# Kernel tuning notes

Measured on AMD Instinct MI355X. Metric: run time of the kernel, lower is better.

## Reference

```python
import jax, jax.numpy as jnp
import numpy as np

EMBED_DIM = 768
NUM_HEADS = 12
LORA_DIM = 64
HEAD_DIM = EMBED_DIM // NUM_HEADS
SCALING = float(HEAD_DIM) ** -0.5


def quick_gelu(x):
    return x * jax.nn.sigmoid(1.702 * x)


def setup_inputs() -> dict:
    key = jax.random.key(0)
    ks = jax.random.split(key, 12)
    bsz, tgt_len, E = 128, 197, EMBED_DIM
    x = jax.random.normal(ks[0], (bsz, tgt_len, E), dtype=jnp.float32)
    attn_mask = jnp.zeros((bsz, tgt_len, tgt_len), dtype=jnp.float32)
    top_idx = jax.random.randint(ks[1], (bsz,), 0, tgt_len)
    s = 0.02
    return {
        "x": x,
        "attn_mask": attn_mask,
        "in_proj_weight": jax.random.normal(ks[2], (3 * E, E)) * s,
        "in_proj_bias": jnp.zeros((3 * E,), jnp.float32),
        "out_proj_weight": jax.random.normal(ks[3], (E, E)) * s,
        "out_proj_bias": jnp.zeros((E,), jnp.float32),
        "lora_a": jax.random.normal(ks[4], (LORA_DIM, E)) * s,
        "lora_b": jax.random.normal(ks[5], (3 * E, LORA_DIM)) * s,
        "down_weight": jax.random.normal(ks[6], (LORA_DIM, E)) * s,
        "down_bias": jax.random.normal(ks[7], (LORA_DIM,)) * 1e-6,
        "up_weight": jax.random.normal(ks[8], (E, LORA_DIM)) * s,
        "up_bias": jnp.zeros((E,), jnp.float32),
        "n_f": 16,
        "top_idx": top_idx,
    }


def reference(x, attn_mask, in_proj_weight, in_proj_bias, out_proj_weight,
              out_proj_bias, lora_a, lora_b, down_weight, down_bias,
              up_weight, up_bias, n_f, top_idx):
    bsz, tgt_len, E = x.shape
    H, hd = NUM_HEADS, HEAD_DIM
    b = bsz // n_f

    # fused QKV + LoRA delta
    qkv = x @ in_proj_weight.T + in_proj_bias          # [bsz, L, 3E]
    qkv = qkv + (x @ lora_a.T) @ lora_b.T              # LoRA delta
    qkv = qkv.reshape(bsz, tgt_len, 3, H, hd)
    qkv = jnp.transpose(qkv, (2, 0, 3, 1, 4))          # [3, bsz, H, L, hd]
    q, k, v = qkv[0], qkv[1], qkv[2]

    # gather per-sample CLS query before scaling (matches torch order)
    q_1 = q[jnp.arange(bsz), :, top_idx, :]            # [bsz, H, hd]
    q_1 = jnp.transpose(q_1.reshape(b, n_f, H, hd), (0, 2, 1, 3))  # [b, H, f, hd]

    # frame-local attention
    attn = jnp.einsum('bhqd,bhkd->bhqk', q * SCALING, k) + attn_mask[:, None, :, :]
    attn = jax.nn.softmax(attn, axis=-1)
    xo = jnp.einsum('bhqk,bhkd->bhqd', attn, v)
    xo = jnp.transpose(xo, (0, 2, 1, 3)).reshape(bsz, tgt_len, E)
    xo = xo @ out_proj_weight.T + out_proj_bias        # [bsz, L, E]

    # global CLS attention over all frames' keys/values
    k_g = jnp.transpose(k.reshape(b, n_f, H, tgt_len, hd), (0, 2, 1, 3, 4)).reshape(b, H, n_f * tgt_len, hd)
    v_g = jnp.transpose(v.reshape(b, n_f, H, tgt_len, hd), (0, 2, 1, 3, 4)).reshape(b, H, n_f * tgt_len, hd)
    mask_g = attn_mask[:, -1, :].reshape(b, n_f * tgt_len)  # [b, f*L]

    attn_1 = jnp.einsum('bhfd,bhkd->bhfk', q_1 * SCALING, k_g) + mask_g[:, None, None, :]
    attn_1 = jax.nn.softmax(attn_1, axis=-1)
    x_1 = jnp.einsum('bhfk,bhkd->bhfd', attn_1, v_g)
    x_1 = jnp.transpose(x_1, (0, 2, 1, 3)).reshape(b, n_f, E)
    x_1 = x_1 @ out_proj_weight.T + out_proj_bias      # [b, f, E]

    # adapter on gathered CLS outputs
    x_0 = xo[jnp.arange(bsz), top_idx, :].reshape(b, n_f, E)
    x_0 = quick_gelu(x_0 @ down_weight.T + down_bias)
    x_0 = x_0 @ up_weight.T + up_bias                  # [b, f, E]

    update_cls = (x_0 + x_1).reshape(bsz, E)
    xo = xo.at[jnp.arange(bsz), top_idx, :].set(update_cls)
    return xo
```

## Files before the change

kernel.cpp:

```cpp
#include <hip/hip_runtime.h>
#include <hip/hip_bf16.h>

typedef __attribute__((ext_vector_type(4))) float f32x4;
typedef __attribute__((ext_vector_type(8))) short s16x8;

#define BSZ 128
#define TGT 197
#define EDIM 768
#define NH 12
#define HD 64
#define NF 16
#define M_TOT (BSZ*TGT)
#define QKV_N (3*EDIM)
#define KG (NF*TGT)
#define KGP 3328
#define VSTR 264

__device__ __forceinline__ float b2f(unsigned short u) {
  return __uint_as_float(((unsigned int)u) << 16);
}
__device__ __forceinline__ float bf2f(__hip_bfloat16 b) { return __bfloat162float(b); }
__device__ __forceinline__ __hip_bfloat16 f2bf(float f) { return __float2bfloat16(f); }
__device__ __forceinline__ unsigned int packbf(float a, float b) {
  __hip_bfloat16 x = __float2bfloat16(a), y = __float2bfloat16(b);
  return (unsigned int)*(unsigned short*)&x | ((unsigned int)*(unsigned short*)&y << 16);
}
__device__ __forceinline__ int swz(int t, int c) {
  return t*64 + (c ^ ((((t & 7) ^ ((t >> 3) & 3))) << 3));
}
__device__ __forceinline__ int vswz(int d, int t) {
  return d*VSTR + (t ^ (d & 56));
}

__device__ __forceinline__ void gload_lds16(const void* gsrc, void* ldst) {
  __builtin_amdgcn_global_load_lds(
      (const __attribute__((address_space(1))) unsigned int*)gsrc,
      (__attribute__((address_space(3))) unsigned int*)ldst, 16, 0, 0);
}

__global__ void detect_dtype(const unsigned short* __restrict__ xraw,
                             int* __restrict__ flag, int* __restrict__ mz) {
  if (threadIdx.x == 0 && blockIdx.x == 0) {
    float mx = 0.f;
    for (int j = 0; j < 1024; ++j) {
      float v = fabsf(b2f(xraw[j]));
      if (v < 1e30f) mx = fmaxf(mx, v);
      else mx = 1e30f;
    }
    *flag = (mx < 100.0f) ? 1 : 0;
    *mz = 1;
  }
}

__global__ __launch_bounds__(256) void detect_mask_zero(
    const unsigned int* __restrict__ mraw, int nelem,
    const int* __restrict__ flag, int* __restrict__ mz)
{
  const int isbf = *flag;
  const int nwords = isbf ? (nelem >> 1) : nelem;
  const unsigned int am = isbf ? 0x7fff7fffu : 0x7fffffffu;
  unsigned int acc = 0;
  for (int i = blockIdx.x*256 + threadIdx.x; i < nwords; i += gridDim.x*256)
    acc |= (mraw[i] & am);
  if (acc) atomicAnd(mz, 0);
}

__global__ __launch_bounds__(256) void convert_bf16(
    const void* __restrict__ src, __hip_bfloat16* __restrict__ dst,
    int n8, const int* __restrict__ flag, int skip_if_bf)
{
  const int isbf = *flag;
  if (skip_if_bf && isbf) return;
  int i = blockIdx.x * 256 + threadIdx.x;
  const int stride = gridDim.x * 256;
  if (isbf) {
    const s16x8* s = (const s16x8*)src;
    s16x8* d = (s16x8*)dst;
    for (; i < n8; i += stride) d[i] = s[i];
  } else {
    const f32x4* s = (const f32x4*)src;
    s16x8* d = (s16x8*)dst;
    for (; i < n8; i += stride) {
      f32x4 a = s[i*2], b = s[i*2+1];
      s16x8 o;
      #pragma unroll
      for (int j = 0; j < 4; ++j) { __hip_bfloat16 t = f2bf(a[j]); o[j] = *(short*)&t; }
      #pragma unroll
      for (int j = 0; j < 4; ++j) { __hip_bfloat16 t = f2bf(b[j]); o[4+j] = *(short*)&t; }
      d[i] = o;
    }
  }
}

struct CvBatch {
  const void* src[10];
  void* dst[10];
  int off8[11];
};

__global__ __launch_bounds__(256) void convert_batch(CvBatch cb, const int* __restrict__ flag)
{
  const int isbf = *flag;
  const int total = cb.off8[10];
  for (int i = blockIdx.x*256 + threadIdx.x; i < total; i += gridDim.x*256) {
    int s = 0;
    #pragma unroll
    for (int k = 1; k < 10; ++k) s += (i >= cb.off8[k]);
    const int li = i - cb.off8[s];
    if (isbf) {
      ((s16x8*)cb.dst[s])[li] = ((const s16x8*)cb.src[s])[li];
    } else {
      const f32x4* sp = (const f32x4*)cb.src[s];
      f32x4 a = sp[li*2], b = sp[li*2+1];
      s16x8 o;
      #pragma unroll
      for (int j = 0; j < 4; ++j) { __hip_bfloat16 t = f2bf(a[j]); o[j] = *(short*)&t; }
      #pragma unroll
      for (int j = 0; j < 4; ++j) { __hip_bfloat16 t = f2bf(b[j]); o[4+j] = *(short*)&t; }
      ((s16x8*)cb.dst[s])[li] = o;
    }
  }
}

__global__ __launch_bounds__(256) void build_wc(
    const __hip_bfloat16* __restrict__ W,
    const __hip_bfloat16* __restrict__ la,
    const __hip_bfloat16* __restrict__ lb,
    __hip_bfloat16* __restrict__ Wc)
{
  __shared__ float lbr[64];
  const int n = blockIdx.x;
  if (threadIdx.x < 64) lbr[threadIdx.x] = bf2f(lb[n*64 + threadIdx.x]);
  __syncthreads();
  for (int e = threadIdx.x; e < EDIM; e += 256) {
    float acc = bf2f(W[(size_t)n*EDIM + e]);
    for (int r = 0; r < 64; ++r) acc += lbr[r] * bf2f(la[r*EDIM + e]);
    Wc[(size_t)n*EDIM + e] = f2bf(acc);
  }
}

__global__ __launch_bounds__(512) void gemm_bt_8ph(
    const __hip_bfloat16* __restrict__ A,
    const __hip_bfloat16* __restrict__ A_alt,
    const __hip_bfloat16* __restrict__ B,
    const __hip_bfloat16* __restrict__ bias,
    void* __restrict__ C,
    int M, int N, int K, int ntiles,
    const int* __restrict__ flag, int flag_mode)
{
  __shared__ char lds[131072];
  const int tid = threadIdx.x;
  const int wave = tid >> 6, lane = tid & 63;
  const int l16 = lane & 15, kq = lane >> 4;
  const int wr = wave >> 2, wc2 = wave & 3;

  const int nwg = gridDim.x;
  const int bid = blockIdx.x;
  const int qc = nwg >> 3, rc = nwg & 7;
  const int xcd = bid & 7;
  const int wgid = (xcd < rc ? xcd*(qc+1) : rc*(qc+1) + (xcd-rc)*qc) + (bid >> 3);
  const long brow = (long)(wgid / ntiles) * 256;
  const long bcol = (long)(wgid % ntiles) * 256;

  const int isbf = *flag;
  const __hip_bfloat16* Ause = isbf ? A_alt : A;
  const int nkt = K >> 6;

  const int srow = tid >> 3;
  const int schunk = tid & 7;
  const int wuni = wave << 10;

  auto stA = [&](int t, int buf, int issue) {
    int ar = issue*64 + srow;
    int cs = schunk ^ (ar & 7);
    long gr = brow + ar; if (gr > (long)M - 1) gr = M - 1;
    gload_lds16(Ause + gr*(long)K + t*64 + cs*8,
                lds + buf*65536 + issue*8192 + wuni);
  };
  auto stB = [&](int t, int buf, int issue) {
    int br = issue*64 + srow;
    int cs = schunk ^ (br & 7);
    gload_lds16(B + (bcol + br)*(long)K + t*64 + cs*8,
                lds + buf*65536 + 32768 + issue*8192 + wuni);
  };
  auto rdA = [&](int buf, int q, int a, int ks) -> s16x8 {
    int ar = wr*128 + q*32 + a*16 + l16;
    int ch = ks*4 + kq;
    return *(const s16x8*)(lds + buf*65536 + ar*128 + ((ch ^ (ar & 7)) << 4));
  };
  auto rdB = [&](int buf, int ni, int ks) -> s16x8 {
    int br = wc2*64 + ni*16 + l16;
    int ch = ks*4 + kq;
    return *(const s16x8*)(lds + buf*65536 + 32768 + br*128 + ((ch ^ (br & 7)) << 4));
  };

  f32x4 acc[8][4];
  #pragma unroll
  for (int i = 0; i < 8; ++i)
    #pragma unroll
    for (int j = 0; j < 4; ++j) acc[i][j] = (f32x4){0.f,0.f,0.f,0.f};

  stB(0,0,0); stB(0,0,1); stB(0,0,2); stB(0,0,3);
  stA(0,0,0); stA(0,0,2); stA(0,0,1); stA(0,0,3);
  asm volatile("s_waitcnt vmcnt(2)" ::: "memory");
  __builtin_amdgcn_s_barrier();

  for (int t = 0; t < nkt; ++t) {
    const int cur = t & 1, nxt = cur ^ 1;
    const bool pf = (t + 1 < nkt);
    s16x8 bfr[4][2], af[2][2];

    #pragma unroll
    for (int ni = 0; ni < 4; ++ni) { bfr[ni][0] = rdB(cur,ni,0); bfr[ni][1] = rdB(cur,ni,1); }
    af[0][0]=rdA(cur,0,0,0); af[0][1]=rdA(cur,0,0,1);
    af[1][0]=rdA(cur,0,1,0); af[1][1]=rdA(cur,0,1,1);
    if (pf) {
      stB(t+1,nxt,0); stB(t+1,nxt,1); stB(t+1,nxt,2); stB(t+1,nxt,3);
      stA(t+1,nxt,0); stA(t+1,nxt,2); stA(t+1,nxt,1); stA(t+1,nxt,3);
    }
    __builtin_amdgcn_s_barrier();
    asm volatile("s_waitcnt lgkmcnt(0)" ::: "memory");
    __builtin_amdgcn_sched_barrier(0);
    __builtin_amdgcn_s_setprio(1);
    #pragma unroll
    for (int ks = 0; ks < 2; ++ks)
      #pragma unroll
      for (int ni = 0; ni < 4; ++ni) {
        acc[0][ni] = __builtin_amdgcn_mfma_f32_16x16x32_bf16(af[0][ks], bfr[ni][ks], acc[0][ni], 0,0,0);
        acc[1][ni] = __builtin_amdgcn_mfma_f32_16x16x32_bf16(af[1][ks], bfr[ni][ks], acc[1][ni], 0,0,0);
      }
    __builtin_amdgcn_s_setprio(0);

    af[0][0]=rdA(cur,1,0,0); af[0][1]=rdA(cur,1,0,1);
    af[1][0]=rdA(cur,1,1,0); af[1][1]=rdA(cur,1,1,1);
    if (pf) asm volatile("s_waitcnt vmcnt(8)" ::: "memory");
    else    asm volatile("s_waitcnt vmcnt(0)" ::: "memory");
    __builtin_amdgcn_s_barrier();
    asm volatile("s_waitcnt lgkmcnt(0)" ::: "memory");
    __builtin_amdgcn_sched_barrier(0);
    __builtin_amdgcn_s_setprio(1);
    #pragma unroll
    for (int ks = 0; ks < 2; ++ks)
      #pragma unroll
      for (int ni = 0; ni < 4; ++ni) {
        acc[2][ni] = __builtin_amdgcn_mfma_f32_16x16x32_bf16(af[0][ks], bfr[ni][ks], acc[2][ni], 0,0,0);
        acc[3][ni] = __builtin_amdgcn_mfma_f32_16x16x32_bf16(af[1][ks], bfr[ni][ks], acc[3][ni], 0,0,0);
      }
    __builtin_amdgcn_s_setprio(0);

    af[0][0]=rdA(cur,2,0,0); af[0][1]=rdA(cur,2,0,1);
    af[1][0]=rdA(cur,2,1,0); af[1][1]=rdA(cur,2,1,1);
    __builtin_amdgcn_s_barrier();
    asm volatile("s_waitcnt lgkmcnt(0)" ::: "memory");
    __builtin_amdgcn_sched_barrier(0);
    __builtin_amdgcn_s_setprio(1);
    #pragma unroll
    for (int ks = 0; ks < 2; ++ks)
      #pragma unroll
      for (int ni = 0; ni < 4; ++ni) {
        acc[4][ni] = __builtin_amdgcn_mfma_f32_16x16x32_bf16(af[0][ks], bfr[ni][ks], acc[4][ni], 0,0,0);
        acc[5][ni] = __builtin_amdgcn_mfma_f32_16x16x32_bf16(af[1][ks], bfr[ni][ks], acc[5][ni], 0,0,0);
      }
    __builtin_amdgcn_s_setprio(0);

    af[0][0]=rdA(cur,3,0,0); af[0][1]=rdA(cur,3,0,1);
    af[1][0]=rdA(cur,3,1,0); af[1][1]=rdA(cur,3,1,1);
    if (pf) asm volatile("s_waitcnt vmcnt(2)" ::: "memory");
    __builtin_amdgcn_s_barrier();
    asm volatile("s_waitcnt lgkmcnt(0)" ::: "memory");
    __builtin_amdgcn_sched_barrier(0);
    __builtin_amdgcn_s_setprio(1);
    #pragma unroll
    for (int ks = 0; ks < 2; ++ks)
      #pragma unroll
      for (int ni = 0; ni < 4; ++ni) {
        acc[6][ni] = __builtin_amdgcn_mfma_f32_16x16x32_bf16(af[0][ks], bfr[ni][ks], acc[6][ni], 0,0,0);
        acc[7][ni] = __builtin_amdgcn_mfma_f32_16x16x32_bf16(af[1][ks], bfr[ni][ks], acc[7][ni], 0,0,0);
      }
    __builtin_amdgcn_s_setprio(0);
  }

  __builtin_amdgcn_s_barrier();

  const int f32o = flag_mode && (!isbf);
  float bv[4];
  #pragma unroll
  for (int ni = 0; ni < 4; ++ni) bv[ni] = bf2f(bias[bcol + wc2*64 + ni*16 + l16]);
  const int o4 = kq*4;

  if (!f32o) {
    __hip_bfloat16* eb = (__hip_bfloat16*)(lds + wave*2048);
    __hip_bfloat16* Cb = (__hip_bfloat16*)C;
    const int rr = lane >> 3, cg = lane & 7;
    #pragma unroll
    for (int mi = 0; mi < 8; ++mi) {
      #pragma unroll
      for (int ni = 0; ni < 4; ++ni)
        #pragma unroll
        for (int r = 0; r < 4; ++r) {
          const int row16 = o4 + r;
          const int sidx = row16*64 + ((((ni*2 + (l16 >> 3)) ^ (row16 & 7)) << 3) | (l16 & 7));
          eb[sidx] = f2bf(acc[mi][ni][r] + bv[ni]);
        }
      asm volatile("s_waitcnt lgkmcnt(0)" ::: "memory");
      __builtin_amdgcn_sched_barrier(0);
      #pragma unroll
      for (int pass = 0; pass < 2; ++pass) {
        const int row16 = pass*8 + rr;
        const long grow = brow + wr*128 + mi*16 + row16;
        if (grow < M) {
          s16x8 v = *(const s16x8*)(eb + row16*64 + ((cg ^ (row16 & 7)) << 3));
          *(s16x8*)(Cb + grow*(long)N + bcol + wc2*64 + cg*8) = v;
        }
      }
      asm volatile("s_waitcnt lgkmcnt(0)" ::: "memory");
      __builtin_amdgcn_sched_barrier(0);
    }
  } else {
    #pragma unroll
    for (int mi = 0; mi < 8; ++mi)
      #pragma unroll
      for (int ni = 0; ni < 4; ++ni)
        #pragma unroll
        for (int r = 0; r < 4; ++r) {
          const long grow = brow + wr*128 + mi*16 + o4 + r;
          if (grow < M)
            ((float*)C)[grow*(long)N + bcol + wc2*64 + ni*16 + l16] = acc[mi][ni][r] + bv[ni];
        }
  }
}

__global__ __launch_bounds__(256) void attn_fused(
    const __hip_bfloat16* __restrict__ qkv,
    const __hip_bfloat16* __restrict__ mask,
    const __hip_bfloat16* __restrict__ mask_raw,
    const int* __restrict__ flag,
    const int* __restrict__ mzp,
    __hip_bfloat16* __restrict__ xop)
{
  __shared__ __hip_bfloat16 lVt[64*VSTR];

  const int tid = threadIdx.x;
  const int blk = blockIdx.x;
  const int xcd = blk & 7;
  const int slot = blk >> 3;
  const int ih = xcd * 192 + (slot >> 2);
  const int qt = slot & 3;
  const int h = ih % NH;
  const int i = ih / NH;
  const int q0 = qt * 64;
  const size_t rowbase = (size_t)i * TGT;
  const int wave = tid >> 6, lane = tid & 63;
  const int l16 = lane & 15, kq = lane >> 4;
  const int mz = *mzp;
  const __hip_bfloat16* msk = (*flag) ? mask_raw : mask;

  int qr = q0 + wave*16 + l16;
  const int qrc = qr > TGT-1 ? TGT-1 : qr;
  s16x8 qf[2];
  #pragma unroll
  for (int kk = 0; kk < 2; ++kk)
    qf[kk] = *(const s16x8*)(qkv + (rowbase + qrc)*QKV_N + h*HD + kk*32 + kq*8);

  const f32x4 z = {0.f,0.f,0.f,0.f};
  for (int idx = tid; idx < 224*8; idx += 256) {
    int t = idx >> 3, c8 = idx & 7;
    f32x4 vv = z;
    if (t < TGT) vv = *(const f32x4*)(qkv + (rowbase + t)*QKV_N + 2*EDIM + h*HD + c8*8);
    const __hip_bfloat16* pv = (const __hip_bfloat16*)&vv;
    const int tx = t ^ (c8 << 3);
    #pragma unroll
    for (int j = 0; j < 8; ++j)
      lVt[(c8*8 + j)*VSTR + tx] = pv[j];
  }
  __syncthreads();

  f32x4 acc[14];
  #pragma unroll
  for (int nf = 0; nf < 14; ++nf) {
    int trow = nf*16 + l16; if (trow > TGT-1) trow = TGT-1;
    acc[nf] = (f32x4){0.f,0.f,0.f,0.f};
    #pragma unroll
    for (int kk = 0; kk < 2; ++kk) {
      s16x8 kf = *(const s16x8*)(qkv + (rowbase + trow)*QKV_N + EDIM + h*HD + kk*32 + kq*8);
      acc[nf] = __builtin_amdgcn_mfma_f32_16x16x32_bf16(kf, qf[kk], acc[nf], 0, 0, 0);
    }
  }

  float mx = -1e30f;
  #pragma unroll
  for (int nf = 0; nf < 14; ++nf) {
    #pragma unroll
    for (int r = 0; r < 4; ++r) {
      const int t = nf*16 + kq*4 + r;
      float s;
      if (t < TGT) {
        s = acc[nf][r]*0.125f;
        if (!mz) s += bf2f(msk[(rowbase + qrc)*TGT + t]);
      } else s = -1e30f;
      acc[nf][r] = s;
      mx = fmaxf(mx, s);
    }
  }
  mx = fmaxf(mx, __shfl_xor(mx, 16));
  mx = fmaxf(mx, __shfl_xor(mx, 32));

  float rs = 0.f;
  unsigned int pk[14][2];
  #pragma unroll
  for (int nf = 0; nf < 14; ++nf) {
    float p0 = __expf(acc[nf][0] - mx);
    float p1 = __expf(acc[nf][1] - mx);
    float p2 = __expf(acc[nf][2] - mx);
    float p3 = __expf(acc[nf][3] - mx);
    rs += (p0 + p1) + (p2 + p3);
    pk[nf][0] = packbf(p0, p1);
    pk[nf][1] = packbf(p2, p3);
  }
  rs += __shfl_xor(rs, 16);
  rs += __shfl_xor(rs, 32);

  f32x4 oacc[4];
  #pragma unroll
  for (int nf = 0; nf < 4; ++nf) oacc[nf] = (f32x4){0.f,0.f,0.f,0.f};

  const int slbase = l16 + ((kq & 1) << 5);
  #pragma unroll
  for (int kt = 0; kt < 7; ++kt) {
    s16x8 pa;
    #pragma unroll
    for (int jp = 0; jp < 4; ++jp) {
      const int srcLane = slbase + ((jp >> 1) << 4);
      int va = __shfl((int)pk[2*kt][jp & 1], srcLane, 64);
      int vb = __shfl((int)pk[2*kt + 1][jp & 1], srcLane, 64);
      int sel = (kq < 2) ? va : vb;
      pa[2*jp]     = (short)(sel & 0xffff);
      pa[2*jp + 1] = (short)(((unsigned int)sel) >> 16);
    }
    #pragma unroll
    for (int nf = 0; nf < 4; ++nf) {
      s16x8 vf = *(const s16x8*)(lVt + vswz(nf*16 + l16, kt*32 + kq*8));
      oacc[nf] = __builtin_amdgcn_mfma_f32_16x16x32_bf16(pa, vf, oacc[nf], 0, 0, 0);
    }
  }

  #pragma unroll
  for (int r = 0; r < 4; ++r) {
    const float rsrc = __shfl(rs, kq*4 + r, 64);
    const int qw = q0 + wave*16 + kq*4 + r;
    if (qw < TGT) {
      const float inv = 1.0f / rsrc;
      #pragma unroll
      for (int nf = 0; nf < 4; ++nf)
        xop[(rowbase + qw)*(size_t)EDIM + h*HD + nf*16 + l16] = f2bf(oacc[nf][r] * inv);
    }
  }
}

__global__ __launch_bounds__(256) void cls_attn(
    const __hip_bfloat16* __restrict__ qkv,
    const __hip_bfloat16* __restrict__ mask,
    const __hip_bfloat16* __restrict__ mask_raw,
    const int* __restrict__ flag,
    const int* __restrict__ mzp,
    const int* __restrict__ top_idx,
    __hip_bfloat16* __restrict__ Sg_all,
    __hip_bfloat16* __restrict__ x1buf)
{
  __shared__ __hip_bfloat16 lQ[16*64];
  __shared__ __hip_bfloat16 lV[256*64];
  __shared__ float red[16][17];
  __shared__ float rmax[16];
  __shared__ float rsum[16];

  const int tid = threadIdx.x;
  const int g = blockIdx.x / NH;
  const int h = blockIdx.x % NH;
  __hip_bfloat16* Sg = Sg_all + (size_t)blockIdx.x * 16 * KGP;
  const int wave = tid >> 6, lane = tid & 63;
  const int l16 = lane & 15, kq = lane >> 4, o4 = (lane >> 4) * 4;
  const int mz = *mzp;
  const __hip_bfloat16* msk = (*flag) ? mask_raw : mask;

  if (tid < 128) {
    int qi = tid >> 3, c8 = tid & 7;
    int ib = g*NF + qi;
    int top = top_idx[ib];
    f32x4 v = *(const f32x4*)(qkv + ((size_t)ib*TGT + top)*QKV_N + h*HD + c8*8);
    *(f32x4*)(lQ + qi*64 + c8*8) = v;
  }
  __syncthreads();

  s16x8 q8[2];
  #pragma unroll
  for (int kk = 0; kk < 2; ++kk)
    q8[kk] = *(const s16x8*)(lQ + l16*64 + kk*32 + kq*8);

  for (int nf = wave; nf < 208; nf += 4) {
    const int key = nf*16 + l16;
    if (nf < 197) {
      f32x4 a = {0.f,0.f,0.f,0.f};
      const size_t krow = (size_t)g*KG + key;
      #pragma unroll
      for (int kk = 0; kk < 2; ++kk) {
        s16x8 k8 = *(const s16x8*)(qkv + krow*QKV_N + EDIM + h*HD + kk*32 + kq*8);
        a = __builtin_amdgcn_mfma_f32_16x16x32_bf16(q8[kk], k8, a, 0, 0, 0);
      }
      float mval = 0.f;
      if (!mz) {
        const int f = key / 197;
        const int t = key - f*197;
        mval = bf2f(msk[((size_t)(g*NF + f)*TGT + (TGT-1))*TGT + t]);
      }
      #pragma unroll
      for (int r = 0; r < 4; ++r)
        Sg[(o4 + r)*KGP + key] = f2bf(a[r]*0.125f + mval);
    } else {
      #pragma unroll
      for (int r = 0; r < 4; ++r)
        Sg[(o4 + r)*KGP + key] = f2bf(0.f);
    }
  }
  __syncthreads();

  {
    const int q = tid >> 4, c = tid & 15;
    float mx = -1e30f;
    for (int gch = c; gch < 394; gch += 16) {
      s16x8 sv = *(const s16x8*)(Sg + q*KGP + gch*8);
      #pragma unroll
      for (int j = 0; j < 8; ++j) mx = fmaxf(mx, b2f((unsigned short)sv[j]));
    }
    red[q][c] = mx;
    __syncthreads();
    if (tid < 16) {
      float m = red[tid][0];
      for (int j = 1; j < 16; ++j) m = fmaxf(m, red[tid][j]);
      rmax[tid] = m;
    }
    __syncthreads();
    const float rowmax = rmax[q];
    float sum = 0.f;
    for (int gch = c; gch < 394; gch += 16) {
      s16x8 sv = *(const s16x8*)(Sg + q*KGP + gch*8);
      s16x8 ov;
      #pragma unroll
      for (int jp = 0; jp < 4; ++jp) {
        float e0 = __expf(b2f((unsigned short)sv[2*jp])   - rowmax);
        float e1 = __expf(b2f((unsigned short)sv[2*jp+1]) - rowmax);
        sum += e0 + e1;
        unsigned int pr = packbf(e0, e1);
        ov[2*jp]   = (short)(pr & 0xffff);
        ov[2*jp+1] = (short)(pr >> 16);
      }
      *(s16x8*)(Sg + q*KGP + gch*8) = ov;
    }
    red[q][c] = sum;
    __syncthreads();
    if (tid < 16) {
      float s = 0.f;
      for (int j = 0; j < 16; ++j) s += red[tid][j];
      rsum[tid] = s;
    }
  }

  f32x4 oa = {0.f,0.f,0.f,0.f};
  const f32x4 z = {0.f,0.f,0.f,0.f};
  for (int ck = 0; ck < KGP; ck += 256) {
    __syncthreads();
    for (int idx = tid; idx < 256*8; idx += 256) {
      int t2 = idx >> 3, c8 = idx & 7;
      int key = ck + t2;
      f32x4 v = z;
      if (key < KG) v = *(const f32x4*)(qkv + ((size_t)g*KG + key)*QKV_N + 2*EDIM + h*HD + c8*8);
      *(f32x4*)(lV + swz(t2, c8*8)) = v;
    }
    __syncthreads();
    #pragma unroll
    for (int ks = 0; ks < 8; ++ks) {
      s16x8 pa = *(const s16x8*)(Sg + l16*KGP + ck + ks*32 + kq*8);
      s16x8 vf;
      #pragma unroll
      for (int j = 0; j < 8; ++j) {
        const int t2 = ks*32 + kq*8 + j;
        vf[j] = *(const short*)(lV + swz(t2, wave*16 + l16));
      }
      oa = __builtin_amdgcn_mfma_f32_16x16x32_bf16(pa, vf, oa, 0, 0, 0);
    }
  }
  #pragma unroll
  for (int r = 0; r < 4; ++r) {
    int q = o4 + r;
    int ib = g*NF + q;
    x1buf[(size_t)ib*EDIM + h*HD + wave*16 + l16] = f2bf(oa[r] / rsum[q]);
  }
}

__global__ __launch_bounds__(256) void final_update(
    void* __restrict__ out,
    const __hip_bfloat16* __restrict__ x1p,
    const __hip_bfloat16* __restrict__ dw, const __hip_bfloat16* __restrict__ db,
    const __hip_bfloat16* __restrict__ uw, const __hip_bfloat16* __restrict__ ub,
    const int* __restrict__ top_idx, const int* __restrict__ flag)
{
  __shared__ float x0[EDIM];
  __shared__ float hmid[64];
  const int i = blockIdx.x;
  const int tid = threadIdx.x;
  const int top = top_idx[i];
  const int isbf = *flag;
  const size_t rowoff = ((size_t)i*TGT + top)*EDIM;
  for (int e = tid; e < EDIM; e += 256)
    x0[e] = isbf ? bf2f(((const __hip_bfloat16*)out)[rowoff + e])
                 : ((const float*)out)[rowoff + e];
  __syncthreads();
  if (tid < 64) {
    float a = bf2f(db[tid]);
    for (int e = 0; e < EDIM; ++e) a += x0[e] * bf2f(dw[tid*EDIM + e]);
    hmid[tid] = a / (1.f + __expf(-1.702f * a));
  }
  __syncthreads();
  for (int e = tid; e < EDIM; e += 256) {
    float a = bf2f(ub[e]) + bf2f(x1p[(size_t)i*EDIM + e]);
    #pragma unroll
    for (int r = 0; r < 64; ++r) a += hmid[r] * bf2f(uw[e*64 + r]);
    if (isbf) ((__hip_bfloat16*)out)[rowoff + e] = f2bf(a);
    else ((float*)out)[rowoff + e] = a;
  }
}

extern "C" void kernel_launch(void* const* d_in, const int* in_sizes, int n_in,
                              void* d_out, int out_size, void* d_ws, size_t ws_size,
                              hipStream_t stream) {
  (void)in_sizes; (void)n_in; (void)out_size; (void)ws_size;
  const int* top_idx = (const int*)d_in[13];
  const __hip_bfloat16* x_raw    = (const __hip_bfloat16*)d_in[0];
  const __hip_bfloat16* mask_raw = (const __hip_bfloat16*)d_in[1];

  char* ws = (char*)d_ws;
  size_t off = 0;
  auto alloc = [&](size_t bytes) { char* p = ws + off; off += (bytes + 15) & ~(size_t)15; return p; };

  int* flag = (int*)alloc(16);
  int* mz   = (int*)alloc(16);
  __hip_bfloat16* x_c    = (__hip_bfloat16*)alloc((size_t)19365888*2);
  __hip_bfloat16* mask_c = (__hip_bfloat16*)alloc((size_t)4967552*2);
  __hip_bfloat16* wIn_c  = (__hip_bfloat16*)alloc((size_t)1769472*2);
  __hip_bfloat16* bIn_c  = (__hip_bfloat16*)alloc((size_t)2304*2);
  __hip_bfloat16* wOut_c = (__hip_bfloat16*)alloc((size_t)589824*2);
  __hip_bfloat16* bOut_c = (__hip_bfloat16*)alloc((size_t)768*2);
  __hip_bfloat16* la_c   = (__hip_bfloat16*)alloc((size_t)49152*2);
  __hip_bfloat16* lb_c   = (__hip_bfloat16*)alloc((size_t)147456*2);
  __hip_bfloat16* dw_c   = (__hip_bfloat16*)alloc((size_t)49152*2);
  __hip_bfloat16* db_c   = (__hip_bfloat16*)alloc((size_t)64*2);
  __hip_bfloat16* uw_c   = (__hip_bfloat16*)alloc((size_t)49152*2);
  __hip_bfloat16* ub_c   = (__hip_bfloat16*)alloc((size_t)768*2);
  __hip_bfloat16* Wc     = (__hip_bfloat16*)alloc((size_t)QKV_N*EDIM*2);
  __hip_bfloat16* qkv    = (__hip_bfloat16*)alloc((size_t)M_TOT*QKV_N*2);
  __hip_bfloat16* xop    = (__hip_bfloat16*)alloc((size_t)M_TOT*EDIM*2);
  __hip_bfloat16* x1b    = (__hip_bfloat16*)alloc((size_t)BSZ*EDIM*2);
  __hip_bfloat16* x1p    = (__hip_bfloat16*)alloc((size_t)BSZ*EDIM*2);
  __hip_bfloat16* Sg     = (__hip_bfloat16*)alloc((size_t)96*16*KGP*2);

  detect_dtype<<<1, 64, 0, stream>>>((const unsigned short*)d_in[0], flag, mz);
  detect_mask_zero<<<2048, 256, 0, stream>>>((const unsigned int*)d_in[1], 4967552, flag, mz);

  convert_bf16<<<2048, 256, 0, stream>>>(d_in[0], x_c, 19365888/8, flag, 1);
  convert_bf16<<<2048, 256, 0, stream>>>(d_in[1], mask_c, 4967552/8, flag, 1);

  CvBatch cb;
  const int srcIdx[10] = {2,3,4,5,6,7,8,9,10,11};
  void* dsts[10] = {wIn_c, bIn_c, wOut_c, bOut_c, la_c, lb_c, dw_c, db_c, uw_c, ub_c};
  const int ns[10] = {1769472, 2304, 589824, 768, 49152, 147456, 49152, 64, 49152, 768};
  int cum = 0;
  for (int k = 0; k < 10; ++k) {
    cb.src[k] = d_in[srcIdx[k]];
    cb.dst[k] = dsts[k];
    cb.off8[k] = cum;
    cum += ns[k] / 8;
  }
  cb.off8[10] = cum;
  convert_batch<<<(cum + 255)/256, 256, 0, stream>>>(cb, flag);

  build_wc<<<2304, 256, 0, stream>>>(wIn_c, la_c, lb_c, Wc);

  gemm_bt_8ph<<<99*9, 512, 0, stream>>>(x_c, x_raw, Wc, bIn_c, qkv,
                                        M_TOT, QKV_N, EDIM, 9, flag, 0);
  attn_fused<<<dim3(6144), 256, 0, stream>>>(qkv, mask_c, mask_raw, flag, mz, xop);
  gemm_bt_8ph<<<99*3, 512, 0, stream>>>(xop, xop, wOut_c, bOut_c, d_out,
                                        M_TOT, EDIM, EDIM, 3, flag, 1);
  cls_attn<<<dim3(96), 256, 0, stream>>>(qkv, mask_c, mask_raw, flag, mz, top_idx, Sg, x1b);
  gemm_bt_8ph<<<1*3, 512, 0, stream>>>(x1b, x1b, wOut_c, bOut_c, x1p,
                                       BSZ, EDIM, EDIM, 3, flag, 0);
  final_update<<<128, 256, 0, stream>>>(d_out, x1p, dw_c, db_c, uw_c, ub_c, top_idx, flag);
}
```

Before: 561.9 us.

## Split CLS global attention across key chunks and stagger GEMM prefetch loads

The global CLS attention, previously 96 blocks each scanning 3152 keys through a global scratch score buffer, is split into 8 key chunks per (group, head). Each chunk keeps its scores in LDS and writes partial max/sum/output, and a new combine kernel merges them flash-decoding style. This raises parallelism from 96 to 768 blocks and removes the global Sg round-trip, at the cost of an extra launch and partial buffers. Separately, the GEMM main loop now spreads its next-tile global-to-LDS loads across the four phases and adjusts the vmcnt waits accordingly.

Result: faster. 469.9 us (-16.4%).

```diff
diff --git a/kernel.cpp b/kernel.cpp
--- a/kernel.cpp
+++ b/kernel.cpp
@@ -13,8 +13,10 @@
 #define M_TOT (BSZ*TGT)
 #define QKV_N (3*EDIM)
 #define KG (NF*TGT)
-#define KGP 3328
 #define VSTR 264
+#define NSPL 8
+#define KSPL 394
+#define LSTR 424
 
 __device__ __forceinline__ float b2f(unsigned short u) {
   return __uint_as_float(((unsigned int)u) << 16);
@@ -214,10 +216,7 @@
     for (int ni = 0; ni < 4; ++ni) { bfr[ni][0] = rdB(cur,ni,0); bfr[ni][1] = rdB(cur,ni,1); }
     af[0][0]=rdA(cur,0,0,0); af[0][1]=rdA(cur,0,0,1);
     af[1][0]=rdA(cur,0,1,0); af[1][1]=rdA(cur,0,1,1);
-    if (pf) {
-      stB(t+1,nxt,0); stB(t+1,nxt,1); stB(t+1,nxt,2); stB(t+1,nxt,3);
-      stA(t+1,nxt,0); stA(t+1,nxt,2); stA(t+1,nxt,1); stA(t+1,nxt,3);
-    }
+    if (pf) { stB(t+1,nxt,0); stB(t+1,nxt,1); }
     __builtin_amdgcn_s_barrier();
     asm volatile("s_waitcnt lgkmcnt(0)" ::: "memory");
     __builtin_amdgcn_sched_barrier(0);
@@ -233,8 +232,12 @@
 
     af[0][0]=rdA(cur,1,0,0); af[0][1]=rdA(cur,1,0,1);
     af[1][0]=rdA(cur,1,1,0); af[1][1]=rdA(cur,1,1,1);
-    if (pf) asm volatile("s_waitcnt vmcnt(8)" ::: "memory");
-    else    asm volatile("s_waitcnt vmcnt(0)" ::: "memory");
+    if (pf) {
+      stB(t+1,nxt,2); stB(t+1,nxt,3);
+      asm volatile("s_waitcnt vmcnt(4)" ::: "memory");
+    } else {
+      asm volatile("s_waitcnt vmcnt(0)" ::: "memory");
+    }
     __builtin_amdgcn_s_barrier();
     asm volatile("s_waitcnt lgkmcnt(0)" ::: "memory");
     __builtin_amdgcn_sched_barrier(0);
@@ -250,6 +253,7 @@
 
     af[0][0]=rdA(cur,2,0,0); af[0][1]=rdA(cur,2,0,1);
     af[1][0]=rdA(cur,2,1,0); af[1][1]=rdA(cur,2,1,1);
+    if (pf) { stA(t+1,nxt,0); stA(t+1,nxt,2); }
     __builtin_amdgcn_s_barrier();
     asm volatile("s_waitcnt lgkmcnt(0)" ::: "memory");
     __builtin_amdgcn_sched_barrier(0);
@@ -265,7 +269,8 @@
 
     af[0][0]=rdA(cur,3,0,0); af[0][1]=rdA(cur,3,0,1);
     af[1][0]=rdA(cur,3,1,0); af[1][1]=rdA(cur,3,1,1);
-    if (pf) asm volatile("s_waitcnt vmcnt(2)" ::: "memory");
+    if (pf) { stA(t+1,nxt,1); stA(t+1,nxt,3); }
+    asm volatile("s_waitcnt vmcnt(2)" ::: "memory");
     __builtin_amdgcn_s_barrier();
     asm volatile("s_waitcnt lgkmcnt(0)" ::: "memory");
     __builtin_amdgcn_sched_barrier(0);
@@ -457,26 +462,30 @@
   }
 }
 
-__global__ __launch_bounds__(256) void cls_attn(
+__global__ __launch_bounds__(256) void cls_split(
     const __hip_bfloat16* __restrict__ qkv,
     const __hip_bfloat16* __restrict__ mask,
     const __hip_bfloat16* __restrict__ mask_raw,
     const int* __restrict__ flag,
     const int* __restrict__ mzp,
     const int* __restrict__ top_idx,
-    __hip_bfloat16* __restrict__ Sg_all,
-    __hip_bfloat16* __restrict__ x1buf)
+    float* __restrict__ pO,
+    float* __restrict__ pm,
+    float* __restrict__ pl)
 {
   __shared__ __hip_bfloat16 lQ[16*64];
+  __shared__ __hip_bfloat16 lS[16*LSTR];
   __shared__ __hip_bfloat16 lV[256*64];
   __shared__ float red[16][17];
   __shared__ float rmax[16];
   __shared__ float rsum[16];
 
   const int tid = threadIdx.x;
-  const int g = blockIdx.x / NH;
-  const int h = blockIdx.x % NH;
-  __hip_bfloat16* Sg = Sg_all + (size_t)blockIdx.x * 16 * KGP;
+  const int sp = blockIdx.x & 7;
+  const int gh = blockIdx.x >> 3;
+  const int g = gh / NH;
+  const int h = gh % NH;
+  const int k0 = sp * KSPL;
   const int wave = tid >> 6, lane = tid & 63;
   const int l16 = lane & 15, kq = lane >> 4, o4 = (lane >> 4) * 4;
   const int mz = *mzp;
@@ -496,38 +505,33 @@
   for (int kk = 0; kk < 2; ++kk)
     q8[kk] = *(const s16x8*)(lQ + l16*64 + kk*32 + kq*8);
 
-  for (int nf = wave; nf < 208; nf += 4) {
-    const int key = nf*16 + l16;
-    if (nf < 197) {
-      f32x4 a = {0.f,0.f,0.f,0.f};
-      const size_t krow = (size_t)g*KG + key;
-      #pragma unroll
-      for (int kk = 0; kk < 2; ++kk) {
-        s16x8 k8 = *(const s16x8*)(qkv + krow*QKV_N + EDIM + h*HD + kk*32 + kq*8);
-        a = __builtin_amdgcn_mfma_f32_16x16x32_bf16(q8[kk], k8, a, 0, 0, 0);
-      }
-      float mval = 0.f;
-      if (!mz) {
-        const int f = key / 197;
-        const int t = key - f*197;
-        mval = bf2f(msk[((size_t)(g*NF + f)*TGT + (TGT-1))*TGT + t]);
-      }
-      #pragma unroll
-      for (int r = 0; r < 4; ++r)
-        Sg[(o4 + r)*KGP + key] = f2bf(a[r]*0.125f + mval);
-    } else {
-      #pragma unroll
-      for (int r = 0; r < 4; ++r)
-        Sg[(o4 + r)*KGP + key] = f2bf(0.f);
-    }
+  for (int nf = wave; nf < 26; nf += 4) {
+    const int keyl = nf*16 + l16;
+    const int keyg = k0 + (keyl < KSPL ? keyl : 0);
+    f32x4 a = {0.f,0.f,0.f,0.f};
+    const size_t krow = (size_t)g*KG + keyg;
+    #pragma unroll
+    for (int kk = 0; kk < 2; ++kk) {
+      s16x8 k8 = *(const s16x8*)(qkv + krow*QKV_N + EDIM + h*HD + kk*32 + kq*8);
+      a = __builtin_amdgcn_mfma_f32_16x16x32_bf16(q8[kk], k8, a, 0, 0, 0);
+    }
+    float mval = 0.f;
+    if (!mz && keyl < KSPL) {
+      const int f = keyg / 197;
+      const int t = keyg - f*197;
+      mval = bf2f(msk[((size_t)(g*NF + f)*TGT + (TGT-1))*TGT + t]);
+    }
+    #pragma unroll
+    for (int r = 0; r < 4; ++r)
+      lS[(o4 + r)*LSTR + nf*16 + l16] = f2bf(keyl < KSPL ? a[r]*0.125f + mval : -1e30f);
   }
   __syncthreads();
 
   {
     const int q = tid >> 4, c = tid & 15;
     float mx = -1e30f;
-    for (int gch = c; gch < 394; gch += 16) {
-      s16x8 sv = *(const s16x8*)(Sg + q*KGP + gch*8);
+    for (int gch = c; gch < 52; gch += 16) {
+      s16x8 sv = *(const s16x8*)(lS + q*LSTR + gch*8);
       #pragma unroll
       for (int j = 0; j < 8; ++j) mx = fmaxf(mx, b2f((unsigned short)sv[j]));
     }
@@ -541,8 +545,8 @@
     __syncthreads();
     const float rowmax = rmax[q];
     float sum = 0.f;
-    for (int gch = c; gch < 394; gch += 16) {
-      s16x8 sv = *(const s16x8*)(Sg + q*KGP + gch*8);
+    for (int gch = c; gch < 52; gch += 16) {
+      s16x8 sv = *(const s16x8*)(lS + q*LSTR + gch*8);
       s16x8 ov;
       #pragma unroll
       for (int jp = 0; jp < 4; ++jp) {
@@ -553,7 +557,7 @@
         ov[2*jp]   = (short)(pr & 0xffff);
         ov[2*jp+1] = (short)(pr >> 16);
       }
-      *(s16x8*)(Sg + q*KGP + gch*8) = ov;
+      *(s16x8*)(lS + q*LSTR + gch*8) = ov;
     }
     red[q][c] = sum;
     __syncthreads();
@@ -566,19 +570,23 @@
 
   f32x4 oa = {0.f,0.f,0.f,0.f};
   const f32x4 z = {0.f,0.f,0.f,0.f};
-  for (int ck = 0; ck < KGP; ck += 256) {
+  #pragma unroll
+  for (int cki = 0; cki < 2; ++cki) {
+    const int ck = cki * 256;
+    const int nrows = cki ? 160 : 256;
+    const int nks = cki ? 5 : 8;
     __syncthreads();
-    for (int idx = tid; idx < 256*8; idx += 256) {
+    for (int idx = tid; idx < nrows*8; idx += 256) {
       int t2 = idx >> 3, c8 = idx & 7;
-      int key = ck + t2;
+      int keyl = ck + t2;
       f32x4 v = z;
-      if (key < KG) v = *(const f32x4*)(qkv + ((size_t)g*KG + key)*QKV_N + 2*EDIM + h*HD + c8*8);
+      if (keyl < KSPL)
+        v = *(const f32x4*)(qkv + ((size_t)g*KG + k0 + keyl)*QKV_N + 2*EDIM + h*HD + c8*8);
       *(f32x4*)(lV + swz(t2, c8*8)) = v;
     }
     __syncthreads();
-    #pragma unroll
-    for (int ks = 0; ks < 8; ++ks) {
-      s16x8 pa = *(const s16x8*)(Sg + l16*KGP + ck + ks*32 + kq*8);
+    for (int ks = 0; ks < nks; ++ks) {
+      s16x8 pa = *(const s16x8*)(lS + l16*LSTR + ck + ks*32 + kq*8);
       s16x8 vf;
       #pragma unroll
       for (int j = 0; j < 8; ++j) {
@@ -588,11 +596,54 @@
       oa = __builtin_amdgcn_mfma_f32_16x16x32_bf16(pa, vf, oa, 0, 0, 0);
     }
   }
-  #pragma unroll
-  for (int r = 0; r < 4; ++r) {
-    int q = o4 + r;
-    int ib = g*NF + q;
-    x1buf[(size_t)ib*EDIM + h*HD + wave*16 + l16] = f2bf(oa[r] / rsum[q]);
+
+  const int ps = gh*NSPL + sp;
+  #pragma unroll
+  for (int r = 0; r < 4; ++r)
+    pO[((size_t)ps*16 + (o4 + r))*64 + wave*16 + l16] = oa[r];
+  if (tid < 16) {
+    pm[ps*16 + tid] = rmax[tid];
+    pl[ps*16 + tid] = rsum[tid];
+  }
+}
+
+__global__ __launch_bounds__(256) void cls_combine(
+    const float* __restrict__ pO,
+    const float* __restrict__ pm,
+    const float* __restrict__ pl,
+    __hip_bfloat16* __restrict__ x1buf)
+{
+  __shared__ float M[16];
+  __shared__ float L[16];
+  __shared__ float sc[NSPL][16];
+  const int tid = threadIdx.x;
+  const int gh = blockIdx.x;
+  const int g = gh / NH;
+  const int h = gh % NH;
+
+  if (tid < 16) {
+    float m = -1e30f;
+    for (int s = 0; s < NSPL; ++s) m = fmaxf(m, pm[(gh*NSPL + s)*16 + tid]);
+    M[tid] = m;
+  }
+  __syncthreads();
+  if (tid < 128) {
+    const int s = tid >> 4, q = tid & 15;
+    sc[s][q] = __expf(pm[(gh*NSPL + s)*16 + q] - M[q]);
+  }
+  __syncthreads();
+  if (tid < 16) {
+    float l = 0.f;
+    for (int s = 0; s < NSPL; ++s) l += pl[(gh*NSPL + s)*16 + tid] * sc[s][tid];
+    L[tid] = l;
+  }
+  __syncthreads();
+  for (int idx = tid; idx < 16*64; idx += 256) {
+    const int q = idx >> 6, d = idx & 63;
+    float acc = 0.f;
+    for (int s = 0; s < NSPL; ++s)
+      acc += pO[((size_t)(gh*NSPL + s)*16 + q)*64 + d] * sc[s][q];
+    x1buf[((size_t)(g*NF + q))*EDIM + h*64 + d] = f2bf(acc / L[q]);
   }
 }
 
@@ -660,7 +711,9 @@
   __hip_bfloat16* xop    = (__hip_bfloat16*)alloc((size_t)M_TOT*EDIM*2);
   __hip_bfloat16* x1b    = (__hip_bfloat16*)alloc((size_t)BSZ*EDIM*2);
   __hip_bfloat16* x1p    = (__hip_bfloat16*)alloc((size_t)BSZ*EDIM*2);
-  __hip_bfloat16* Sg     = (__hip_bfloat16*)alloc((size_t)96*16*KGP*2);
+  float* pO = (float*)alloc((size_t)96*NSPL*16*64*4);
+  float* pm = (float*)alloc((size_t)96*NSPL*16*4);
+  float* pl = (float*)alloc((size_t)96*NSPL*16*4);
 
   detect_dtype<<<1, 64, 0, stream>>>((const unsigned short*)d_in[0], flag, mz);
   detect_mask_zero<<<2048, 256, 0, stream>>>((const unsigned int*)d_in[1], 4967552, flag, mz);
@@ -687,10 +740,12 @@
   gemm_bt_8ph<<<99*9, 512, 0, stream>>>(x_c, x_raw, Wc, bIn_c, qkv,
                                         M_TOT, QKV_N, EDIM, 9, flag, 0);
   attn_fused<<<dim3(6144), 256, 0, stream>>>(qkv, mask_c, mask_raw, flag, mz, xop);
+  cls_split<<<dim3(96*NSPL), 256, 0, stream>>>(qkv, mask_c, mask_raw, flag, mz,
+                                               top_idx, pO, pm, pl);
   gemm_bt_8ph<<<99*3, 512, 0, stream>>>(xop, xop, wOut_c, bOut_c, d_out,
                                         M_TOT, EDIM, EDIM, 3, flag, 1);
-  cls_attn<<<dim3(96), 256, 0, stream>>>(qkv, mask_c, mask_raw, flag, mz, top_idx, Sg, x1b);
-  gemm_bt_8ph<<<1*3, 512, 0, stream>>>(x1b, x1b, wOut_c, bOut_c, x1p,
-                                       BSZ, EDIM, EDIM, 3, flag, 0);
+  cls_combine<<<dim3(96), 256, 0, stream>>>(pO, pm, pl, x1b);
+  gemm_bt_8ph<<<3, 512, 0, stream>>>(x1b, x1b, wOut_c, bOut_c, x1p,
+                                     BSZ, EDIM, EDIM, 3, flag, 0);
   final_update<<<128, 256, 0, stream>>>(d_out, x1p, dw_c, db_c, uw_c, ub_c, top_idx, flag);
 }
```
